# Performance work log

Measured on AMD Instinct MI355X. Metric: run time of the kernel, lower is better.

## Reference

```python
import jax, jax.numpy as jnp
import numpy as np

# dims matching init_kwargs
L, D, NH = 4, 1024, 16          # num_blocks, embed_dim, num_heads
HD = D // NH                     # head dim
CUR, MEM, BS, IN = 512, 512, 8, 512
FF = 4 * D
GRU_BIAS = 2.0

def sinusoidal_pe(full_seq, dim):
    # SinusoidalPE: freqs = arange(0, dim, 2); inv = 10000**(-freqs/dim); seq descending
    freqs = jnp.arange(0, dim, 2.0)
    inv = 10000.0 ** (-freqs / dim)
    seq = jnp.arange(full_seq - 1, -1, -1.0)
    ang = seq[:, None] * inv[None, :]                       # (full, dim/2)
    return jnp.concatenate([jnp.sin(ang), jnp.cos(ang)], axis=-1)  # (full, dim)

def layer_norm(x, g, b, eps=1e-5):
    m = x.mean(-1, keepdims=True)
    v = ((x - m) ** 2).mean(-1, keepdims=True)
    return (x - m) * jax.lax.rsqrt(v + eps) * g + b

def rel_shift(x):
    # Transformer-XL relative shift. x: (q, k, b, h)
    q, k, b, h = x.shape
    zp = jnp.zeros((q, 1, b, h), x.dtype)
    return jnp.concatenate([zp, x], axis=1).reshape(k + 1, q, b, h)[1:].reshape(q, k, b, h)

def gru_gate(x, y, W):
    # W: (6, D, D) = Wr, Ur, Wz, Uz, Wg, Ug (no bias except learned-ish gru_bias on z)
    Wr, Ur, Wz, Uz, Wg, Ug = W[0], W[1], W[2], W[3], W[4], W[5]
    r = jax.nn.sigmoid(y @ Wr.T + x @ Ur.T)
    z = jax.nn.sigmoid(y @ Wz.T + x @ Uz.T - GRU_BIAS)
    hh = jnp.tanh(y @ Wg.T + (r * x) @ Ug.T)
    return (1.0 - z) * x + z * hh

def rel_attn(q, k, v, pos, U, V, mask, W):
    # q: (cur, bs, D); k, v: (full, bs, D); pos: (full, D); W: (5, D, D) = Wq,Wk,Wv,Wr,Wo
    cur, bs, _ = q.shape
    full = k.shape[0]
    qh = (q @ W[0].T).reshape(cur, bs, NH, HD)
    kh = (k @ W[1].T).reshape(full, bs, NH, HD)
    vh = (v @ W[2].T).reshape(full, bs, NH, HD)
    rh = (pos @ W[3].T).reshape(full, NH, HD)
    AC = jnp.einsum('ibhd,jbhd->ijbh', qh + U, kh)          # content stream with U bias
    BD = rel_shift(jnp.einsum('ibhd,jhd->ijbh', qh + V, rh))  # position stream with V bias
    score = (AC + BD) * (1.0 / np.sqrt(HD))
    score = jnp.where(mask[:, :, None, None], jnp.asarray(-1e30, score.dtype), score)
    attn = jax.nn.softmax(score, axis=1)
    out = jnp.einsum('ijbh,jbhd->ibhd', attn, vh).reshape(cur, bs, D)
    return out @ W[4].T

def gelu(x):
    return jax.nn.gelu(x, approximate=False)  # torch nn.GELU default is exact

def _forward(h, memory, W_emb, b_emb, U, V, ln1, ln2, Wattn, g1, g2, fc_W1, fc_b1, fc_W2, fc_b2):
    h = jnp.transpose(h, (1, 0, 2))            # (cur, bs, in)
    mem = jax.lax.stop_gradient(memory)        # memory holds detached hidden states
    cur = h.shape[0]
    prev = mem.shape[1]
    full = cur + prev
    x = gelu(h @ W_emb.T + b_emb)              # linear embedding + GELU activation
    pos = sinusoidal_pe(full, D)               # (full, D); pos_emb.unsqueeze(1) broadcast over bs
    mask = jnp.triu(jnp.ones((cur, full), bool), 1 + prev)
    out = x
    for i in range(L):
        key = jnp.concatenate([mem[i], out], axis=0)   # (full, bs, D)
        nq = layer_norm(out, ln1[i, 0], ln1[i, 1])
        nk = layer_norm(key, ln1[i, 0], ln1[i, 1])
        Y = rel_attn(nq, nk, nk, pos, U, V, mask, Wattn[i])
        Y = gelu(Y)                                     # dropout is identity (eval / p=0)
        o1 = gru_gate(out, Y, g1[i])
        E = layer_norm(o1, ln2[i, 0], ln2[i, 1])
        E = gelu(gelu(E @ fc_W1[i].T + fc_b1[i]) @ fc_W2[i].T + fc_b2[i])
        out = gru_gate(o1, E, g2[i])
    return jnp.transpose(out, (1, 0, 2))       # (bs, cur, D)

def setup_inputs() -> dict:
    key = jax.random.key(0)
    ks = jax.random.split(key, 12)
    s = 0.02
    eye2 = jnp.stack([jnp.ones(D, jnp.float32), jnp.zeros(D, jnp.float32)])  # (gamma, beta)
    return {
        'h': jax.random.normal(ks[0], (BS, CUR, IN), jnp.float32),
        'memory': jax.random.normal(ks[1], (L, MEM, BS, D), jnp.float32),
        'W_emb': jax.random.normal(ks[2], (D, IN), jnp.float32) * s,
        'b_emb': jnp.zeros((D,), jnp.float32),
        'U': jax.random.normal(ks[3], (NH, HD), jnp.float32) * s,
        'V': jax.random.normal(ks[4], (NH, HD), jnp.float32) * s,
        'ln1': jnp.tile(eye2[None], (L, 1, 1)),
        'ln2': jnp.tile(eye2[None], (L, 1, 1)),
        'Wattn': jax.random.normal(ks[5], (L, 5, D, D), jnp.float32) * s,  # q,k,v,r,o per block
        'g1': jax.random.normal(ks[6], (L, 6, D, D), jnp.float32) * s,
        'g2': jax.random.normal(ks[7], (L, 6, D, D), jnp.float32) * s,
        'fc_W1': jax.random.normal(ks[8], (L, FF, D), jnp.float32) * s,
        'fc_b1': jnp.zeros((L, FF), jnp.float32),
        'fc_W2': jax.random.normal(ks[9], (L, D, FF), jnp.float32) * s,
        'fc_b2': jnp.zeros((L, D), jnp.float32),
    }

def reference(h, memory, W_emb, b_emb, U, V, ln1, ln2, Wattn, g1, g2, fc_W1, fc_b1, fc_W2, fc_b2):
    return _forward(h, memory, W_emb, b_emb, U, V, ln1, ln2, Wattn, g1, g2, fc_W1, fc_b1, fc_W2, fc_b2)
```

## Files before the change

### kernel.cpp

```cpp
#include <hip/hip_runtime.h>
#include <hip/hip_bf16.h>


typedef __attribute__((ext_vector_type(8))) __bf16 bfrag;
typedef __attribute__((ext_vector_type(4))) float f4;
typedef __attribute__((ext_vector_type(4))) unsigned short u16x4;
typedef __attribute__((ext_vector_type(8))) unsigned short u16x8;

__device__ __forceinline__ unsigned short f2bf(float f){
  union { float f; unsigned u; } v; v.f = f;
  unsigned r = v.u + 0x7fffu + ((v.u >> 16) & 1u);
  return (unsigned short)(r >> 16);
}
__device__ __forceinline__ float bf2f(unsigned short u){
  union { unsigned u; float f; } v; v.u = (unsigned)u << 16; return v.f;
}
__device__ __forceinline__ float geluf(float x){
  return 0.5f * x * (1.0f + erff(x * 0.7071067811865476f));
}
__device__ __forceinline__ float sigm(float x){ return 1.0f/(1.0f + __expf(-x)); }

__device__ __forceinline__ void gl_lds(const void* g, void* l){
  __builtin_amdgcn_global_load_lds(
    reinterpret_cast<const __attribute__((address_space(1))) unsigned int*>(
        reinterpret_cast<unsigned long>(g)),
    reinterpret_cast<__attribute__((address_space(3))) unsigned int*>(
        reinterpret_cast<unsigned long>(l)),
    16, 0, 0);
}

struct GP {
  const unsigned short* A;
  const unsigned short* A2;
  const unsigned short* B;
  const unsigned short* B2;
  unsigned short* O1;
  unsigned short* O2;
  unsigned short* O3;
  unsigned short* O4;
  unsigned short* O5;
  float* OF;
  const float* bias1;
  const float* bias2;
  const float* X;
  const float* Z;
  int K, Ksplit, lda, ldb, ldo;
  int sBz;
};

template<int BM, int BN, int EPI>
__global__ __launch_bounds__(256) void gemm_k(GP p){
  __shared__ unsigned short As[BM*32];
  __shared__ unsigned short Bs[BN*32];
  const int tid  = threadIdx.x;
  const int lane = tid & 63;
  const int wid  = tid >> 6;
  const int lr   = lane & 15;
  const int lg   = lane >> 4;
  constexpr int FM = BM/32, FN = BN/32;
  const int m0 = blockIdx.y * BM;
  const int n0 = blockIdx.x * BN;
  const int z  = blockIdx.z;

  const unsigned short* Abase = p.A;
  const unsigned short* Bbase = p.B;
  if constexpr (EPI==13){
    if (z==2){ if (blockIdx.y >= 32) return; Abase = p.A + 4194304; }
    if (z==3){ if (blockIdx.y >= 8)  return; Abase = p.A2; }
    const int zsel = (z==0)?1:((z==1)?2:((z==2)?0:3));
    Bbase = p.B + (long)zsel*1048576;
  }

  const int ksp = p.Ksplit ? p.Ksplit : p.K;
  const unsigned short* AbL = Abase + (long)m0*p.lda;
  const unsigned short* AbH = p.A2 && EPI!=13 ? (p.A2 + (long)m0*p.lda - ksp) : AbL;
  const unsigned short* BbL = Bbase + (long)z*p.sBz + (long)n0*p.ldb;
  const unsigned short* BbH = p.B2 ? (p.B2 + (long)z*p.sBz + (long)n0*p.ldb - ksp) : BbL;

  const int srow = tid >> 2;
  const int skk  = (tid & 3) * 8;

  f4 acc[FM][FN];
  f4 zero4 = {0.0f, 0.0f, 0.0f, 0.0f};
  #pragma unroll
  for (int m=0;m<FM;m++)
    #pragma unroll
    for (int n=0;n<FN;n++) acc[m][n] = zero4;

  for (int k0 = 0; k0 < p.K; k0 += 32){
    const unsigned short* A_ = (k0 < ksp) ? AbL : AbH;
    const unsigned short* B_ = (k0 < ksp) ? BbL : BbH;
    #pragma unroll
    for (int q=0;q<BM/64;q++)
      gl_lds(A_ + (long)(q*64 + srow)*p.lda + k0 + skk, (char*)As + q*4096 + wid*1024);
    #pragma unroll
    for (int q=0;q<BN/64;q++)
      gl_lds(B_ + (long)(q*64 + srow)*p.ldb + k0 + skk, (char*)Bs + q*4096 + wid*1024);
    __syncthreads();
    bfrag af[FM], bfr[FN];
    #pragma unroll
    for (int m=0;m<FM;m++)
      af[m] = *(const bfrag*)&As[((wid>>1)*(BM/2) + m*16 + lr)*32 + lg*8];
    #pragma unroll
    for (int n=0;n<FN;n++)
      bfr[n] = *(const bfrag*)&Bs[((wid&1)*(BN/2) + n*16 + lr)*32 + lg*8];
    #pragma unroll
    for (int m=0;m<FM;m++)
      #pragma unroll
      for (int n=0;n<FN;n++)
        acc[m][n] = __builtin_amdgcn_mfma_f32_16x16x32_bf16(af[m], bfr[n], acc[m][n], 0, 0, 0);
    __syncthreads();
  }

  const int wr0 = m0 + (wid>>1)*(BM/2);
  const int wc0 = n0 + (wid&1)*(BN/2);
  #pragma unroll
  for (int m=0;m<FM;m++)
    #pragma unroll
    for (int n=0;n<FN;n++)
      #pragma unroll
      for (int r=0;r<4;r++){
        const int gr = wr0 + m*16 + lg*4 + r;
        const int gc = wc0 + n*16 + lr;
        const float a = acc[m][n][r];
        const long base = (long)gr*p.ldo + gc;
        if constexpr (EPI==6){
          const float t = a + (p.bias1 ? p.bias1[gc] : 0.0f);
          p.O1[base] = f2bf(geluf(t));
        }
        else if constexpr (EPI==7){
          const float t = geluf(a + p.bias1[gc]);
          p.OF[base] = t; p.O1[base] = f2bf(t);
        }
        else if constexpr (EPI==11){
          const long ix = (long)gr*1024 + gc;
          if (z==0) p.O1[ix] = f2bf(sigm(a) * p.X[ix]);
          else      p.OF[ix] = sigm(a - 2.0f);
        }
        else if constexpr (EPI==12){
          const long ix = (long)gr*1024 + gc;
          const float zz = p.Z[ix];
          const float oo = (1.0f - zz)*p.X[ix] + zz*tanhf(a);
          p.OF[ix] = oo; p.O1[ix] = f2bf(oo);
        }
        else if constexpr (EPI==13){
          const long ix = (long)gr*1024 + gc;
          if (z==0){ p.O1[ix] = f2bf(a); }
          else if (z==1){
            const int b_ = gr & 7, js = gr >> 3, h_ = gc >> 6, d_ = gc & 63;
            p.O2[(long)(b_*16 + h_)*65536 + (long)d_*1024 + js] = f2bf(a);
          }
          else if (z==2){ p.O3[ix] = f2bf(a + p.bias1[gc]); p.O4[ix] = f2bf(a + p.bias2[gc]); }
          else { p.O5[ix] = f2bf(a); }
        }
      }
}

__global__ __launch_bounds__(256) void attn_k(const unsigned short* __restrict__ qU,
                                              const unsigned short* __restrict__ qV,
                                              const unsigned short* __restrict__ kh,
                                              const unsigned short* __restrict__ rh,
                                              const unsigned short* __restrict__ vhT,
                                              unsigned short* __restrict__ ctx){
  __shared__ unsigned short S[32*1024];
  __shared__ float redm[4][32];
  __shared__ float reds[4][32];
  __shared__ float invd[32];
  const int tid = threadIdx.x;
  const int w   = tid >> 6;
  const int lane= tid & 63;
  const int lr  = lane & 15;
  const int lg  = lane >> 4;
  const int id = blockIdx.x;
  const int b  = id & 7;
  const int k5 = id >> 3;
  const int h  = k5 >> 4;
  const int i0 = (k5 & 15) * 32;
  const long qoff = (long)h*64;

  f4 acc[2][16];
  const f4 z4 = {0.f,0.f,0.f,0.f};
  bfrag av[2][2];

  #pragma unroll
  for (int m=0;m<2;m++)
    #pragma unroll
    for (int kk=0;kk<2;kk++)
      av[m][kk] = *(const bfrag*)(qV + ((long)(i0 + m*16 + lr)*8 + b)*1024 + qoff + kk*32 + lg*8);
  #pragma unroll
  for (int m=0;m<2;m++)
    #pragma unroll
    for (int n=0;n<16;n++) acc[m][n] = z4;
  #pragma unroll
  for (int n=0;n<16;n++){
    const long r = w*256 + n*16 + lr;
    bfrag b0 = *(const bfrag*)(rh + r*1024 + qoff + lg*8);
    bfrag b1 = *(const bfrag*)(rh + r*1024 + qoff + 32 + lg*8);
    #pragma unroll
    for (int m=0;m<2;m++){
      acc[m][n] = __builtin_amdgcn_mfma_f32_16x16x32_bf16(av[m][0], b0, acc[m][n],0,0,0);
      acc[m][n] = __builtin_amdgcn_mfma_f32_16x16x32_bf16(av[m][1], b1, acc[m][n],0,0,0);
    }
  }
  #pragma unroll
  for (int m=0;m<2;m++)
    #pragma unroll
    for (int n=0;n<16;n++)
      #pragma unroll
      for (int r4=0;r4<4;r4++){
        const int di = m*16 + lg*4 + r4;
        const int j  = (w*256 + n*16 + lr) + i0 + di - 511;
        if (j >= 0 && j < 1024){
          const int byte = di*2048 + (((j*2) ^ ((di&7)<<4)));
          *(unsigned short*)((char*)S + byte) = f2bf(acc[m][n][r4]);
        }
      }
  __syncthreads();

  #pragma unroll
  for (int m=0;m<2;m++)
    #pragma unroll
    for (int kk=0;kk<2;kk++)
      av[m][kk] = *(const bfrag*)(qU + ((long)(i0 + m*16 + lr)*8 + b)*1024 + qoff + kk*32 + lg*8);
  #pragma unroll
  for (int m=0;m<2;m++)
    #pragma unroll
    for (int n=0;n<16;n++) acc[m][n] = z4;
  #pragma unroll
  for (int n=0;n<16;n++){
    const long j = w*256 + n*16 + lr;
    bfrag b0 = *(const bfrag*)(kh + (j*8 + b)*1024 + qoff + lg*8);
    bfrag b1 = *(const bfrag*)(kh + (j*8 + b)*1024 + qoff + 32 + lg*8);
    #pragma unroll
    for (int m=0;m<2;m++){
      acc[m][n] = __builtin_amdgcn_mfma_f32_16x16x32_bf16(av[m][0], b0, acc[m][n],0,0,0);
      acc[m][n] = __builtin_amdgcn_mfma_f32_16x16x32_bf16(av[m][1], b1, acc[m][n],0,0,0);
    }
  }
  float mx[2][4];
  #pragma unroll
  for (int m=0;m<2;m++)
    #pragma unroll
    for (int r4=0;r4<4;r4++) mx[m][r4] = -3.0e38f;
  #pragma unroll
  for (int m=0;m<2;m++)
    #pragma unroll
    for (int n=0;n<16;n++)
      #pragma unroll
      for (int r4=0;r4<4;r4++){
        const int di = m*16 + lg*4 + r4;
        const int jc = w*256 + n*16 + lr;
        const int byte = di*2048 + (((jc*2) ^ ((di&7)<<4)));
        const float bd = bf2f(*(const unsigned short*)((char*)S + byte));
        float s = (acc[m][n][r4] + bd) * 0.125f;
        s = (jc > i0 + di + 512) ? -1e30f : s;
        acc[m][n][r4] = s;
        mx[m][r4] = fmaxf(mx[m][r4], s);
      }
  #pragma unroll
  for (int m=0;m<2;m++)
    #pragma unroll
    for (int r4=0;r4<4;r4++){
      float v = mx[m][r4];
      v = fmaxf(v, __shfl_xor(v, 1));
      v = fmaxf(v, __shfl_xor(v, 2));
      v = fmaxf(v, __shfl_xor(v, 4));
      v = fmaxf(v, __shfl_xor(v, 8));
      if (lr == 0) redm[w][m*16 + lg*4 + r4] = v;
    }
  __syncthreads();
  float sm[2][4];
  #pragma unroll
  for (int m=0;m<2;m++)
    #pragma unroll
    for (int r4=0;r4<4;r4++){
      const int row = m*16 + lg*4 + r4;
      mx[m][r4] = fmaxf(fmaxf(redm[0][row], redm[1][row]), fmaxf(redm[2][row], redm[3][row]));
      sm[m][r4] = 0.0f;
    }
  #pragma unroll
  for (int m=0;m<2;m++)
    #pragma unroll
    for (int n=0;n<16;n++)
      #pragma unroll
      for (int r4=0;r4<4;r4++){
        const int di = m*16 + lg*4 + r4;
        const int jc = w*256 + n*16 + lr;
        const float e = __expf(acc[m][n][r4] - mx[m][r4]);
        sm[m][r4] += e;
        const int byte = di*2048 + (((jc*2) ^ ((di&7)<<4)));
        *(unsigned short*)((char*)S + byte) = f2bf(e);
      }
  #pragma unroll
  for (int m=0;m<2;m++)
    #pragma unroll
    for (int r4=0;r4<4;r4++){
      float v = sm[m][r4];
      v += __shfl_xor(v, 1);
      v += __shfl_xor(v, 2);
      v += __shfl_xor(v, 4);
      v += __shfl_xor(v, 8);
      if (lr == 0) reds[w][m*16 + lg*4 + r4] = v;
    }
  __syncthreads();
  if (tid < 32)
    invd[tid] = 1.0f / (reds[0][tid] + reds[1][tid] + reds[2][tid] + reds[3][tid]);

  f4 oac[2][4];
  #pragma unroll
  for (int m=0;m<2;m++)
    #pragma unroll
    for (int nd=0;nd<4;nd++) oac[m][nd] = z4;
  const unsigned short* vb_base = vhT + (long)(b*16 + h)*65536;
  #pragma unroll
  for (int jt=0;jt<8;jt++){
    const int jb = w*256 + jt*32;
    bfrag pa[2], vb[4];
    #pragma unroll
    for (int m=0;m<2;m++){
      const int row = m*16 + lr;
      const int cb  = ((jb + lg*8)*2) ^ ((row&7)<<4);
      pa[m] = *(const bfrag*)((char*)S + row*2048 + cb);
    }
    #pragma unroll
    for (int nd=0;nd<4;nd++)
      vb[nd] = *(const bfrag*)(vb_base + (long)(nd*16 + lr)*1024 + jb + lg*8);
    #pragma unroll
    for (int m=0;m<2;m++)
      #pragma unroll
      for (int nd=0;nd<4;nd++)
        oac[m][nd] = __builtin_amdgcn_mfma_f32_16x16x32_bf16(pa[m], vb[nd], oac[m][nd],0,0,0);
  }
  __syncthreads();
  float* po = (float*)S;
  #pragma unroll
  for (int m=0;m<2;m++)
    #pragma unroll
    for (int nd=0;nd<4;nd++)
      #pragma unroll
      for (int r4=0;r4<4;r4++)
        po[w*2048 + (m*16 + lg*4 + r4)*64 + nd*16 + lr] = oac[m][nd][r4];
  __syncthreads();
  {
    const int e0 = tid*8;
    const int row = e0 >> 6;
    const int d0 = e0 & 63;
    float s[8];
    #pragma unroll
    for (int q=0;q<8;q++) s[q] = po[e0 + q];
    #pragma unroll
    for (int ww=1;ww<4;ww++)
      #pragma unroll
      for (int q=0;q<8;q++) s[q] += po[ww*2048 + e0 + q];
    const float inv = invd[row];
    u16x8 o;
    #pragma unroll
    for (int q=0;q<8;q++) o[q] = f2bf(s[q]*inv);
    *(u16x8*)(ctx + ((long)(i0 + row)*8 + b)*1024 + qoff + d0) = o;
  }
}

__global__ __launch_bounds__(256) void ln_k(const float* __restrict__ srcA,
                                            const float* __restrict__ srcB, int splitRow,
                                            const float* __restrict__ g, const float* __restrict__ b,
                                            unsigned short* __restrict__ dst){
  const int row = blockIdx.x;
  const float* src = (srcB != nullptr && row >= splitRow)
                       ? (srcB + (long)(row - splitRow)*1024)
                       : (srcA + (long)row*1024);
  const int t = threadIdx.x;
  float4 v = ((const float4*)src)[t];
  float s1 = v.x+v.y+v.z+v.w;
  float s2 = v.x*v.x+v.y*v.y+v.z*v.z+v.w*v.w;
  #pragma unroll
  for (int o=32;o;o>>=1){ s1 += __shfl_xor(s1,o); s2 += __shfl_xor(s2,o); }
  __shared__ float r1[4], r2[4];
  const int w = t>>6;
  if ((t&63)==0){ r1[w]=s1; r2[w]=s2; }
  __syncthreads();
  s1 = r1[0]+r1[1]+r1[2]+r1[3];
  s2 = r2[0]+r2[1]+r2[2]+r2[3];
  const float mean = s1*(1.0f/1024.0f);
  const float var  = s2*(1.0f/1024.0f) - mean*mean;
  const float rs   = rsqrtf(var + 1e-5f);
  float4 gg = ((const float4*)g)[t];
  float4 bb = ((const float4*)b)[t];
  u16x4 o;
  o.x = f2bf((v.x-mean)*rs*gg.x + bb.x);
  o.y = f2bf((v.y-mean)*rs*gg.y + bb.y);
  o.z = f2bf((v.z-mean)*rs*gg.z + bb.z);
  o.w = f2bf((v.w-mean)*rs*gg.w + bb.w);
  *(u16x4*)(dst + (long)row*1024 + t*4) = o;
}

__global__ __launch_bounds__(256) void conv_k(const float* __restrict__ s,
                                              unsigned short* __restrict__ d, long n){
  long i = ((long)blockIdx.x*256 + threadIdx.x)*4;
  if (i >= n) return;
  float4 v = *(const float4*)(s + i);
  u16x4 o; o.x=f2bf(v.x); o.y=f2bf(v.y); o.z=f2bf(v.z); o.w=f2bf(v.w);
  *(u16x4*)(d + i) = o;
}

__global__ __launch_bounds__(128) void ht_k(const float* __restrict__ h,
                                            unsigned short* __restrict__ d){
  const int row = blockIdx.x;
  const int i = row>>3, b = row&7;
  const float* src = h + ((long)b*512 + i)*512;
  const int t = threadIdx.x;
  float4 v = ((const float4*)src)[t];
  u16x4 o; o.x=f2bf(v.x); o.y=f2bf(v.y); o.z=f2bf(v.z); o.w=f2bf(v.w);
  *(u16x4*)(d + (long)row*512 + t*4) = o;
}

__global__ __launch_bounds__(256) void pos_k(unsigned short* __restrict__ d){
  const int r = blockIdx.x, t = threadIdx.x;
  const float seq = (float)(1023 - r);
  u16x4 o;
  #pragma unroll
  for (int q=0;q<4;q++){
    const int c = t*4 + q;
    const int f = (c < 512) ? c : (c - 512);
    const float inv = expf((float)f * -0.017988946039016f);
    const float ang = seq * inv;
    const float val = (c < 512) ? sinf(ang) : cosf(ang);
    o[q] = f2bf(val);
  }
  *(u16x4*)(d + (long)r*1024 + t*4) = o;
}

__global__ __launch_bounds__(256) void outT_k(const float* __restrict__ o,
                                              float* __restrict__ d){
  const int row = blockIdx.x;
  const int b = row>>9, i = row&511;
  const float4 v = ((const float4*)(o + ((long)i*8 + b)*1024))[threadIdx.x];
  ((float4*)(d + (long)row*1024))[threadIdx.x] = v;
}

extern "C" void kernel_launch(void* const* d_in, const int* in_sizes, int n_in,
                              void* d_out, int out_size, void* d_ws, size_t ws_size,
                              hipStream_t stream){
  (void)in_sizes; (void)n_in; (void)out_size; (void)ws_size;
  const float* h     = (const float*)d_in[0];
  const float* memin = (const float*)d_in[1];
  const float* Wemb  = (const float*)d_in[2];
  const float* bemb  = (const float*)d_in[3];
  const float* Ub    = (const float*)d_in[4];
  const float* Vb    = (const float*)d_in[5];
  const float* ln1   = (const float*)d_in[6];
  const float* ln2   = (const float*)d_in[7];
  const float* Wattn = (const float*)d_in[8];
  const float* g1w   = (const float*)d_in[9];
  const float* g2w   = (const float*)d_in[10];
  const float* fw1   = (const float*)d_in[11];
  const float* fb1   = (const float*)d_in[12];
  const float* fw2   = (const float*)d_in[13];
  const float* fb2   = (const float*)d_in[14];

  char* Wp = (char*)d_ws;
  size_t off = 0;
  auto take = [&](size_t bytes)->size_t{ size_t r = off; off += (bytes + 255) & ~(size_t)255; return r; };
  float*          outf = (float*)         (Wp + take(16777216));
  unsigned short* xbf  = (unsigned short*)(Wp + take( 8388608));
  float*          o1f  = (float*)         (Wp + take(16777216));
  unsigned short* o1b  = (unsigned short*)(Wp + take( 8388608));
  float*          zbf  = (float*)         (Wp + take(16777216));
  unsigned short* rxb  = (unsigned short*)(Wp + take( 8388608));
  unsigned short* yb   = (unsigned short*)(Wp + take( 8388608));
  unsigned short* Eb   = (unsigned short*)(Wp + take( 8388608));
  unsigned short* wb0  = (unsigned short*)(Wp + take(52428800));
  unsigned short* hTb  = (unsigned short*)(Wp + take( 4194304));
  unsigned short* webb = (unsigned short*)(Wp + take( 1048576));
  unsigned short* posb = (unsigned short*)(Wp + take( 2097152));
  unsigned short* nkb  = (unsigned short*)(Wp + take(16777216));
  unsigned short* qUb  = (unsigned short*)(Wp + take( 8388608));
  unsigned short* qVb  = (unsigned short*)(Wp + take( 8388608));
  unsigned short* khb  = (unsigned short*)(Wp + take(16777216));
  unsigned short* vhTb = (unsigned short*)(Wp + take(16777216));
  unsigned short* F1b  = khb;
  unsigned short* rhb  = (unsigned short*)(Wp + take( 2097152));
  unsigned short* ctxb = (unsigned short*)(Wp + take( 8388608));

  const int M1 = 1048576;

  conv_k<<<512, 256, 0, stream>>>(Wemb, webb, 524288);
  ht_k<<<4096, 128, 0, stream>>>(h, hTb);
  pos_k<<<1024, 256, 0, stream>>>(posb);

  {
    GP p{}; p.A=hTb; p.B=webb; p.OF=outf; p.O1=xbf; p.bias1=bemb;
    p.K=512; p.lda=512; p.ldb=512; p.ldo=1024;
    gemm_k<128,128,7><<<dim3(8,32,1),256,0,stream>>>(p);
  }

  auto gru_fn = [&](const unsigned short* xb, const float* xf, const unsigned short* yb_,
                    const unsigned short* w6, float* of, unsigned short* ob){
    { GP p{}; p.A=yb_; p.A2=xb; p.B=w6; p.B2=w6+M1; p.sBz=2*M1;
      p.O1=rxb; p.OF=zbf; p.X=xf;
      p.K=2048; p.Ksplit=1024; p.lda=1024; p.ldb=1024; p.ldo=1024;
      gemm_k<128,128,11><<<dim3(8,32,2),256,0,stream>>>(p); }
    { GP p{}; p.A=yb_; p.A2=rxb; p.B=w6+4*M1; p.B2=w6+5*M1;
      p.X=xf; p.Z=zbf; p.OF=of; p.O1=ob;
      p.K=2048; p.Ksplit=1024; p.lda=1024; p.ldb=1024; p.ldo=1024;
      gemm_k<128,64,12><<<dim3(16,32,1),256,0,stream>>>(p); }
  };

  for (int l = 0; l < 4; ++l){
    conv_k<<<5120,256,0,stream>>>(Wattn + (long)l*5242880, wb0,          5242880);
    conv_k<<<6144,256,0,stream>>>(g1w   + (long)l*6291456, wb0 +  5*M1,  6291456);
    conv_k<<<6144,256,0,stream>>>(g2w   + (long)l*6291456, wb0 + 11*M1,  6291456);
    conv_k<<<4096,256,0,stream>>>(fw1   + (long)l*4194304, wb0 + 17*M1,  4194304);
    conv_k<<<4096,256,0,stream>>>(fw2   + (long)l*4194304, wb0 + 21*M1,  4194304);

    ln_k<<<8192,256,0,stream>>>(memin + (long)l*4194304, outf, 4096,
                                ln1 + l*2048, ln1 + l*2048 + 1024, nkb);

    {
      GP p{}; p.A=nkb; p.A2=posb; p.B=wb0;
      p.O1=khb; p.O2=vhTb; p.O3=qUb; p.O4=qVb; p.O5=rhb;
      p.bias1=Ub; p.bias2=Vb;
      p.K=1024; p.lda=1024; p.ldb=1024; p.ldo=1024;
      gemm_k<128,128,13><<<dim3(8,64,4),256,0,stream>>>(p); }

    attn_k<<<2048,256,0,stream>>>(qUb, qVb, khb, rhb, vhTb, ctxb);

    {
      GP p{}; p.A=ctxb; p.B=wb0+4*M1; p.O1=yb;
      p.K=1024; p.lda=1024; p.ldb=1024; p.ldo=1024;
      gemm_k<128,64,6><<<dim3(16,32,1),256,0,stream>>>(p); }

    gru_fn(xbf, outf, yb, wb0 + 5*M1, o1f, o1b);

    ln_k<<<4096,256,0,stream>>>(o1f, nullptr, 1<<30,
                                ln2 + l*2048, ln2 + l*2048 + 1024, Eb);

    { GP p{}; p.A=Eb;  p.B=wb0+17*M1; p.O1=F1b; p.bias1=fb1 + l*4096;
      p.K=1024; p.lda=1024; p.ldb=1024; p.ldo=4096;
      gemm_k<128,128,6><<<dim3(32,32,1),256,0,stream>>>(p); }
    { GP p{}; p.A=F1b; p.B=wb0+21*M1; p.O1=yb; p.bias1=fb2 + l*1024;
      p.K=4096; p.lda=4096; p.ldb=4096; p.ldo=1024;
      gemm_k<128,64,6><<<dim3(16,32,1),256,0,stream>>>(p); }

    gru_fn(o1b, o1f, yb, wb0 + 11*M1, outf, xbf);
  }

  outT_k<<<4096,256,0,stream>>>(outf, (float*)d_out);
}
```

Baseline: 3.281 ms.

## Restructure relative attention kernel to 16-row tiles with banded positional scores

Rewrites the attention kernel so each block handles 16 query rows instead of 32. Only the band of positional (BD) scores needed after the relative shift is computed, and it is staged in a small LDS buffer. Scores stay in registers, the LDS footprint drops, and a launch bound asks for three blocks per CU, all to raise occupancy. The softmax scale is folded into the q projection epilogue, and the embedding GEMM tile is halved. The trade-off is twice as many blocks, with the K and V loads repeated per 16-row tile, plus extra syncs across the two halves.

```diff
diff --git a/kernel.cpp b/kernel.cpp
--- a/kernel.cpp
+++ b/kernel.cpp
@@ -150,22 +150,23 @@
             const int b_ = gr & 7, js = gr >> 3, h_ = gc >> 6, d_ = gc & 63;
             p.O2[(long)(b_*16 + h_)*65536 + (long)d_*1024 + js] = f2bf(a);
           }
-          else if (z==2){ p.O3[ix] = f2bf(a + p.bias1[gc]); p.O4[ix] = f2bf(a + p.bias2[gc]); }
+          else if (z==2){ p.O3[ix] = f2bf((a + p.bias1[gc])*0.125f);
+                          p.O4[ix] = f2bf((a + p.bias2[gc])*0.125f); }
           else { p.O5[ix] = f2bf(a); }
         }
       }
 }
 
-__global__ __launch_bounds__(256) void attn_k(const unsigned short* __restrict__ qU,
-                                              const unsigned short* __restrict__ qV,
-                                              const unsigned short* __restrict__ kh,
-                                              const unsigned short* __restrict__ rh,
-                                              const unsigned short* __restrict__ vhT,
-                                              unsigned short* __restrict__ ctx){
-  __shared__ unsigned short S[32*1024];
-  __shared__ float redm[4][32];
-  __shared__ float reds[4][32];
-  __shared__ float invd[32];
+__global__ __launch_bounds__(256,3) void attn_k(const unsigned short* __restrict__ qU,
+                                                const unsigned short* __restrict__ qV,
+                                                const unsigned short* __restrict__ kh,
+                                                const unsigned short* __restrict__ rh,
+                                                const unsigned short* __restrict__ vhT,
+                                                unsigned short* __restrict__ ctx){
+  __shared__ char Sm[20480];
+  __shared__ float redm[4][16];
+  __shared__ float reds[4][16];
+  __shared__ float invd[16];
   const int tid = threadIdx.x;
   const int w   = tid >> 6;
   const int lane= tid & 63;
@@ -173,190 +174,155 @@
   const int lg  = lane >> 4;
   const int id = blockIdx.x;
   const int b  = id & 7;
-  const int k5 = id >> 3;
-  const int h  = k5 >> 4;
-  const int i0 = (k5 & 15) * 32;
-  const long qoff = (long)h*64;
-
-  f4 acc[2][16];
+  const int i0 = ((id >> 3) & 31) * 16;
+  const int h  = id >> 8;
+  const long hoff = (long)h * 64;
   const f4 z4 = {0.f,0.f,0.f,0.f};
-  bfrag av[2][2];
-
-  #pragma unroll
-  for (int m=0;m<2;m++)
-    #pragma unroll
-    for (int kk=0;kk<2;kk++)
-      av[m][kk] = *(const bfrag*)(qV + ((long)(i0 + m*16 + lr)*8 + b)*1024 + qoff + kk*32 + lg*8);
-  #pragma unroll
-  for (int m=0;m<2;m++)
-    #pragma unroll
-    for (int n=0;n<16;n++) acc[m][n] = z4;
-  #pragma unroll
-  for (int n=0;n<16;n++){
-    const long r = w*256 + n*16 + lr;
-    bfrag b0 = *(const bfrag*)(rh + r*1024 + qoff + lg*8);
-    bfrag b1 = *(const bfrag*)(rh + r*1024 + qoff + 32 + lg*8);
-    #pragma unroll
-    for (int m=0;m<2;m++){
-      acc[m][n] = __builtin_amdgcn_mfma_f32_16x16x32_bf16(av[m][0], b0, acc[m][n],0,0,0);
-      acc[m][n] = __builtin_amdgcn_mfma_f32_16x16x32_bf16(av[m][1], b1, acc[m][n],0,0,0);
+
+  bfrag bqv[2];
+  #pragma unroll
+  for (int kk=0;kk<2;kk++)
+    bqv[kk] = *(const bfrag*)(qV + ((long)(i0 + lr)*8 + b)*1024 + hoff + kk*32 + lg*8);
+  bfrag aq[2];
+  #pragma unroll
+  for (int kk=0;kk<2;kk++)
+    aq[kk] = *(const bfrag*)(qU + ((long)(i0 + lr)*8 + b)*1024 + hoff + kk*32 + lg*8);
+
+  f4 s[16];
+
+  #pragma unroll
+  for (int half=0; half<2; ++half){
+    const int c0    = half*512;
+    const int rbase = half ? (1008 - i0) : (496 - i0);
+    const int ntil  = half ? (1 + (i0>>4)) : 33;
+    const int radd  = half ? -497 : 15;
+    for (int mt = w; mt < ntil; mt += 4){
+      const int r0 = rbase + mt*16;
+      f4 acc = z4;
+      #pragma unroll
+      for (int kk=0;kk<2;kk++){
+        bfrag ar = *(const bfrag*)(rh + (long)(r0 + lr)*1024 + hoff + kk*32 + lg*8);
+        acc = __builtin_amdgcn_mfma_f32_16x16x32_bf16(ar, bqv[kk], acc, 0,0,0);
+      }
+      #pragma unroll
+      for (int q=0;q<4;q++){
+        const int rr = mt*16 + lg*4 + q;
+        *(unsigned short*)(Sm + rr*32 + ((lr*2) ^ ((rr&15)<<1))) = f2bf(acc[q]);
+      }
     }
-  }
-  #pragma unroll
-  for (int m=0;m<2;m++)
-    #pragma unroll
-    for (int n=0;n<16;n++)
-      #pragma unroll
-      for (int r4=0;r4<4;r4++){
-        const int di = m*16 + lg*4 + r4;
-        const int j  = (w*256 + n*16 + lr) + i0 + di - 511;
-        if (j >= 0 && j < 1024){
-          const int byte = di*2048 + (((j*2) ^ ((di&7)<<4)));
-          *(unsigned short*)((char*)S + byte) = f2bf(acc[m][n][r4]);
+    __syncthreads();
+    const int cw = c0 + w*128;
+    #pragma unroll
+    for (int n=0;n<8;n++){
+      f4 a = z4;
+      #pragma unroll
+      for (int kk=0;kk<2;kk++){
+        bfrag bk = *(const bfrag*)(kh + ((long)(cw + n*16 + lr)*8 + b)*1024 + hoff + kk*32 + lg*8);
+        a = __builtin_amdgcn_mfma_f32_16x16x32_bf16(aq[kk], bk, a, 0,0,0);
+      }
+      #pragma unroll
+      for (int q=0;q<4;q++){
+        const int di = lg*4 + q;
+        const int jc = cw + n*16 + lr;
+        if (jc > i0 + di + 512) a[q] = -1e30f;
+        else {
+          const int rr = jc - di + radd;
+          a[q] += bf2f(*(const unsigned short*)(Sm + rr*32 + (((di*2)) ^ ((rr&15)<<1))));
         }
       }
+      s[half*8 + n] = a;
+    }
+    __syncthreads();
+  }
+
+  float mx[4], sum[4];
+  #pragma unroll
+  for (int q=0;q<4;q++){
+    float m = -3.0e38f;
+    #pragma unroll
+    for (int n=0;n<16;n++) m = fmaxf(m, fmaxf(fmaxf(s[n][q], s[n][q]), s[n][q]));
+    m = s[0][q];
+    #pragma unroll
+    for (int n=1;n<16;n++) m = fmaxf(m, s[n][q]);
+    m = fmaxf(m, __shfl_xor(m, 1));
+    m = fmaxf(m, __shfl_xor(m, 2));
+    m = fmaxf(m, __shfl_xor(m, 4));
+    m = fmaxf(m, __shfl_xor(m, 8));
+    if (lr == 0) redm[w][lg*4+q] = m;
+  }
   __syncthreads();
-
-  #pragma unroll
-  for (int m=0;m<2;m++)
-    #pragma unroll
-    for (int kk=0;kk<2;kk++)
-      av[m][kk] = *(const bfrag*)(qU + ((long)(i0 + m*16 + lr)*8 + b)*1024 + qoff + kk*32 + lg*8);
-  #pragma unroll
-  for (int m=0;m<2;m++)
-    #pragma unroll
-    for (int n=0;n<16;n++) acc[m][n] = z4;
-  #pragma unroll
-  for (int n=0;n<16;n++){
-    const long j = w*256 + n*16 + lr;
-    bfrag b0 = *(const bfrag*)(kh + (j*8 + b)*1024 + qoff + lg*8);
-    bfrag b1 = *(const bfrag*)(kh + (j*8 + b)*1024 + qoff + 32 + lg*8);
-    #pragma unroll
-    for (int m=0;m<2;m++){
-      acc[m][n] = __builtin_amdgcn_mfma_f32_16x16x32_bf16(av[m][0], b0, acc[m][n],0,0,0);
-      acc[m][n] = __builtin_amdgcn_mfma_f32_16x16x32_bf16(av[m][1], b1, acc[m][n],0,0,0);
+  #pragma unroll
+  for (int q=0;q<4;q++){
+    const int row = lg*4+q;
+    mx[q] = fmaxf(fmaxf(redm[0][row], redm[1][row]), fmaxf(redm[2][row], redm[3][row]));
+    sum[q] = 0.0f;
+  }
+  #pragma unroll
+  for (int n=0;n<16;n++)
+    #pragma unroll
+    for (int q=0;q<4;q++){
+      const float e = __expf(s[n][q] - mx[q]);
+      s[n][q] = e;
+      sum[q] += e;
     }
-  }
-  float mx[2][4];
-  #pragma unroll
-  for (int m=0;m<2;m++)
-    #pragma unroll
-    for (int r4=0;r4<4;r4++) mx[m][r4] = -3.0e38f;
-  #pragma unroll
-  for (int m=0;m<2;m++)
-    #pragma unroll
-    for (int n=0;n<16;n++)
-      #pragma unroll
-      for (int r4=0;r4<4;r4++){
-        const int di = m*16 + lg*4 + r4;
-        const int jc = w*256 + n*16 + lr;
-        const int byte = di*2048 + (((jc*2) ^ ((di&7)<<4)));
-        const float bd = bf2f(*(const unsigned short*)((char*)S + byte));
-        float s = (acc[m][n][r4] + bd) * 0.125f;
-        s = (jc > i0 + di + 512) ? -1e30f : s;
-        acc[m][n][r4] = s;
-        mx[m][r4] = fmaxf(mx[m][r4], s);
+  #pragma unroll
+  for (int q=0;q<4;q++){
+    float v = sum[q];
+    v += __shfl_xor(v, 1);
+    v += __shfl_xor(v, 2);
+    v += __shfl_xor(v, 4);
+    v += __shfl_xor(v, 8);
+    if (lr == 0) reds[w][lg*4+q] = v;
+  }
+  __syncthreads();
+  if (tid < 16)
+    invd[tid] = 1.0f / (reds[0][tid] + reds[1][tid] + reds[2][tid] + reds[3][tid]);
+
+  f4 oac[4];
+  #pragma unroll
+  for (int nd=0;nd<4;nd++) oac[nd] = z4;
+  const unsigned short* vb_base = vhT + (long)(b*16 + h)*65536;
+  char* Pch = Sm + w*1024;
+  #pragma unroll
+  for (int t=0;t<8;t++){
+    const int jb = (t < 4) ? (w*128 + t*32) : (512 + w*128 + (t-4)*32);
+    #pragma unroll
+    for (int nn=0;nn<2;nn++){
+      const f4 e = s[2*t + nn];
+      #pragma unroll
+      for (int q=0;q<4;q++){
+        const int row = lg*4 + q;
+        const int col = nn*16 + lr;
+        *(unsigned short*)(Pch + row*64 + ((col*2) ^ (((row>>2)&3)<<4))) = f2bf(e[q]);
       }
-  #pragma unroll
-  for (int m=0;m<2;m++)
-    #pragma unroll
-    for (int r4=0;r4<4;r4++){
-      float v = mx[m][r4];
-      v = fmaxf(v, __shfl_xor(v, 1));
-      v = fmaxf(v, __shfl_xor(v, 2));
-      v = fmaxf(v, __shfl_xor(v, 4));
-      v = fmaxf(v, __shfl_xor(v, 8));
-      if (lr == 0) redm[w][m*16 + lg*4 + r4] = v;
     }
-  __syncthreads();
-  float sm[2][4];
-  #pragma unroll
-  for (int m=0;m<2;m++)
-    #pragma unroll
-    for (int r4=0;r4<4;r4++){
-      const int row = m*16 + lg*4 + r4;
-      mx[m][r4] = fmaxf(fmaxf(redm[0][row], redm[1][row]), fmaxf(redm[2][row], redm[3][row]));
-      sm[m][r4] = 0.0f;
+    bfrag pa = *(const bfrag*)(Pch + lr*64 + ((lg*16) ^ (((lr>>2)&3)<<4)));
+    #pragma unroll
+    for (int nd=0;nd<4;nd++){
+      bfrag bv = *(const bfrag*)(vb_base + (long)(nd*16 + lr)*1024 + jb + lg*8);
+      oac[nd] = __builtin_amdgcn_mfma_f32_16x16x32_bf16(pa, bv, oac[nd], 0,0,0);
     }
-  #pragma unroll
-  for (int m=0;m<2;m++)
-    #pragma unroll
-    for (int n=0;n<16;n++)
-      #pragma unroll
-      for (int r4=0;r4<4;r4++){
-        const int di = m*16 + lg*4 + r4;
-        const int jc = w*256 + n*16 + lr;
-        const float e = __expf(acc[m][n][r4] - mx[m][r4]);
-        sm[m][r4] += e;
-        const int byte = di*2048 + (((jc*2) ^ ((di&7)<<4)));
-        *(unsigned short*)((char*)S + byte) = f2bf(e);
-      }
-  #pragma unroll
-  for (int m=0;m<2;m++)
-    #pragma unroll
-    for (int r4=0;r4<4;r4++){
-      float v = sm[m][r4];
-      v += __shfl_xor(v, 1);
-      v += __shfl_xor(v, 2);
-      v += __shfl_xor(v, 4);
-      v += __shfl_xor(v, 8);
-      if (lr == 0) reds[w][m*16 + lg*4 + r4] = v;
-    }
-  __syncthreads();
-  if (tid < 32)
-    invd[tid] = 1.0f / (reds[0][tid] + reds[1][tid] + reds[2][tid] + reds[3][tid]);
-
-  f4 oac[2][4];
-  #pragma unroll
-  for (int m=0;m<2;m++)
-    #pragma unroll
-    for (int nd=0;nd<4;nd++) oac[m][nd] = z4;
-  const unsigned short* vb_base = vhT + (long)(b*16 + h)*65536;
-  #pragma unroll
-  for (int jt=0;jt<8;jt++){
-    const int jb = w*256 + jt*32;
-    bfrag pa[2], vb[4];
-    #pragma unroll
-    for (int m=0;m<2;m++){
-      const int row = m*16 + lr;
-      const int cb  = ((jb + lg*8)*2) ^ ((row&7)<<4);
-      pa[m] = *(const bfrag*)((char*)S + row*2048 + cb);
-    }
-    #pragma unroll
-    for (int nd=0;nd<4;nd++)
-      vb[nd] = *(const bfrag*)(vb_base + (long)(nd*16 + lr)*1024 + jb + lg*8);
-    #pragma unroll
-    for (int m=0;m<2;m++)
-      #pragma unroll
-      for (int nd=0;nd<4;nd++)
-        oac[m][nd] = __builtin_amdgcn_mfma_f32_16x16x32_bf16(pa[m], vb[nd], oac[m][nd],0,0,0);
-  }
-  __syncthreads();
-  float* po = (float*)S;
-  #pragma unroll
-  for (int m=0;m<2;m++)
-    #pragma unroll
-    for (int nd=0;nd<4;nd++)
-      #pragma unroll
-      for (int r4=0;r4<4;r4++)
-        po[w*2048 + (m*16 + lg*4 + r4)*64 + nd*16 + lr] = oac[m][nd][r4];
+  }
+  float* po = (float*)(Sm + 4096 + w*4096);
+  #pragma unroll
+  for (int nd=0;nd<4;nd++)
+    #pragma unroll
+    for (int q=0;q<4;q++)
+      po[(lg*4+q)*64 + nd*16 + lr] = oac[nd][q];
   __syncthreads();
   {
-    const int e0 = tid*8;
-    const int row = e0 >> 6;
-    const int d0 = e0 & 63;
-    float s[8];
-    #pragma unroll
-    for (int q=0;q<8;q++) s[q] = po[e0 + q];
-    #pragma unroll
-    for (int ww=1;ww<4;ww++)
-      #pragma unroll
-      for (int q=0;q<8;q++) s[q] += po[ww*2048 + e0 + q];
-    const float inv = invd[row];
-    u16x8 o;
-    #pragma unroll
-    for (int q=0;q<8;q++) o[q] = f2bf(s[q]*inv);
-    *(u16x8*)(ctx + ((long)(i0 + row)*8 + b)*1024 + qoff + d0) = o;
+    const int row = tid >> 4;
+    const int d0  = (tid & 15) * 4;
+    f4 v = *(const f4*)(Sm + 4096 + (row*64 + d0)*4);
+    #pragma unroll
+    for (int ww=1;ww<4;ww++){
+      const f4 u = *(const f4*)(Sm + 4096 + ww*4096 + (row*64 + d0)*4);
+      v.x += u.x; v.y += u.y; v.z += u.z; v.w += u.w;
+    }
+    const float iv = invd[row];
+    u16x4 o;
+    o.x = f2bf(v.x*iv); o.y = f2bf(v.y*iv); o.z = f2bf(v.z*iv); o.w = f2bf(v.w*iv);
+    *(u16x4*)(ctx + ((long)(i0 + row)*8 + b)*1024 + hoff + d0) = o;
   }
 }
 
@@ -490,7 +456,7 @@
   {
     GP p{}; p.A=hTb; p.B=webb; p.OF=outf; p.O1=xbf; p.bias1=bemb;
     p.K=512; p.lda=512; p.ldb=512; p.ldo=1024;
-    gemm_k<128,128,7><<<dim3(8,32,1),256,0,stream>>>(p);
+    gemm_k<128,64,7><<<dim3(16,32,1),256,0,stream>>>(p);
   }
 
   auto gru_fn = [&](const unsigned short* xb, const float* xf, const unsigned short* yb_,
@@ -522,7 +488,7 @@
       p.K=1024; p.lda=1024; p.ldb=1024; p.ldo=1024;
       gemm_k<128,128,13><<<dim3(8,64,4),256,0,stream>>>(p); }
 
-    attn_k<<<2048,256,0,stream>>>(qUb, qVb, khb, rhb, vhTb, ctxb);
+    attn_k<<<4096,256,0,stream>>>(qUb, qVb, khb, rhb, vhTb, ctxb);
 
     {
       GP p{}; p.A=ctxb; p.B=wb0+4*M1; p.O1=yb;
```

Result: faster. 3.083 ms (-6.0%).
